# Performance work log

Hardware: AMD Instinct MI355X
Metric: run time of the kernel (lower is better)

The kernel has to match this reference:

```python
import jax, jax.numpy as jnp
import numpy as np
import math

B, H, S, D = 4, 16, 1024, 64
NEG = -1000000000.0

def setup_inputs() -> dict:
    key = jax.random.key(0)
    ks = jax.random.split(key, 6)
    return {
        "query": jax.random.normal(ks[0], (B, H, S, D), dtype=jnp.float32),
        "key": jax.random.normal(ks[1], (B, H, S, D), dtype=jnp.float32),
        "value": jax.random.normal(ks[2], (B, H, S, D), dtype=jnp.float32),
        "head_nums": H,
        "mask": jax.random.randint(ks[3], (B, S), 0, 2, dtype=jnp.int32),
        "topic_query": jax.random.normal(ks[4], (B, S, D), dtype=jnp.float32),
        "topic_key": jax.random.normal(ks[5], (B, S, D), dtype=jnp.float32),
    }

def reference(query, key, value, head_nums, mask, topic_query, topic_key):
    d = query.shape[-1]
    # scores: [B,H,S,S]
    scores = jnp.einsum("bhqd,bhkd->bhqk", query, key) / math.sqrt(d)
    # pairwise mask: [B,S,S] (mask_i * mask_j)
    pair_mask = (mask[:, :, None] * mask[:, None, :]) != 0
    scores = jnp.where(pair_mask[:, None, :, :], scores, NEG)
    # topic modulation: per-token (no head dim), broadcast over heads
    dt = topic_query.shape[-1]
    topic_scores = jnp.einsum("bqd,bkd->bqk", topic_query, topic_key) / math.sqrt(dt)
    topic_scores = jnp.where(pair_mask, topic_scores, 1.0)[:, None, :, :]  # [B,1,S,S]
    topic_probs = jax.nn.softmax(topic_scores, axis=-1)
    scores = scores * topic_probs
    p_attn = jax.nn.softmax(scores, axis=-1)
    out = jnp.einsum("bhqk,bhkd->bhqd", p_attn, value)
    return (out, p_attn)
```

## Files before the change

### kernel.cpp

```cpp
#include <hip/hip_runtime.h>

#define B_ 4
#define H_ 16
#define S_ 1024
#define D_ 64
#define NEGV -1000000000.0f

typedef __bf16 bf16x8 __attribute__((ext_vector_type(8)));
typedef __bf16 bf16x4 __attribute__((ext_vector_type(4)));
typedef float f32x4 __attribute__((ext_vector_type(4)));

__device__ __forceinline__ bf16x8 cvt8(const float* p) {
  float4 x = *(const float4*)p;
  float4 y = *(const float4*)(p + 4);
  bf16x8 f;
  f[0]=(__bf16)x.x; f[1]=(__bf16)x.y; f[2]=(__bf16)x.z; f[3]=(__bf16)x.w;
  f[4]=(__bf16)y.x; f[5]=(__bf16)y.y; f[6]=(__bf16)y.z; f[7]=(__bf16)y.w;
  return f;
}

__global__ __launch_bounds__(256) void prep_kernel(
    const float* __restrict__ K, const float* __restrict__ V,
    __bf16* __restrict__ Kb, __bf16* __restrict__ Vt)
{
  int bid = blockIdx.x;
  int sc = bid & 15;
  int bh = bid >> 4;
  int tid = threadIdx.x;
  __shared__ float s_v[64][65];

  const float* Kc = K + ((size_t)bh*S_ + sc*64)*D_;
  const float* Vc = V + ((size_t)bh*S_ + sc*64)*D_;
  __bf16* Kbc = Kb + ((size_t)bh*S_ + sc*64)*D_;

  {
    const float4* src = (const float4*)Kc + tid*4;
    float4 a = src[0], b = src[1], c = src[2], d = src[3];
    bf16x8 o0, o1;
    o0[0]=(__bf16)a.x; o0[1]=(__bf16)a.y; o0[2]=(__bf16)a.z; o0[3]=(__bf16)a.w;
    o0[4]=(__bf16)b.x; o0[5]=(__bf16)b.y; o0[6]=(__bf16)b.z; o0[7]=(__bf16)b.w;
    o1[0]=(__bf16)c.x; o1[1]=(__bf16)c.y; o1[2]=(__bf16)c.z; o1[3]=(__bf16)c.w;
    o1[4]=(__bf16)d.x; o1[5]=(__bf16)d.y; o1[6]=(__bf16)d.z; o1[7]=(__bf16)d.w;
    *(bf16x8*)(Kbc + tid*16)     = o0;
    *(bf16x8*)(Kbc + tid*16 + 8) = o1;
  }
  for (int i = tid; i < 64*16; i += 256) {
    int r = i >> 4, c4 = i & 15;
    float4 v = ((const float4*)(Vc + (size_t)r*D_))[c4];
    s_v[r][c4*4+0] = v.x; s_v[r][c4*4+1] = v.y;
    s_v[r][c4*4+2] = v.z; s_v[r][c4*4+3] = v.w;
  }
  __syncthreads();
  {
    int d = tid >> 2, seg = tid & 3;
    bf16x8 o0, o1;
    #pragma unroll
    for (int j = 0; j < 8; ++j) o0[j] = (__bf16)s_v[seg*16 + j][d];
    #pragma unroll
    for (int j = 0; j < 8; ++j) o1[j] = (__bf16)s_v[seg*16 + 8 + j][d];
    __bf16* dst = Vt + ((size_t)bh*D_ + d)*S_ + sc*64 + seg*16;
    *(bf16x8*)dst = o0;
    *(bf16x8*)(dst + 8) = o1;
  }
}

__global__ __launch_bounds__(256) void topic_kernel(
    const float* __restrict__ tq, const float* __restrict__ tk,
    const int* __restrict__ mask, float* __restrict__ tp)
{
  int bid0 = blockIdx.x;
  int bid = (bid0 & 7)*32 + (bid0 >> 3);
  int qt = bid & 63, b = bid >> 6;
  int tid = threadIdx.x, wave = tid >> 6, lane = tid & 63;
  int l15 = lane & 15, lhi = lane >> 4;
  __shared__ float2 s_red[4][16];
  __shared__ __align__(16) char s_mem[4*8704];

  const int* mb = mask + b*S_;
  bf16x8 qf[2];
  #pragma unroll
  for (int dc = 0; dc < 2; ++dc)
    qf[dc] = cvt8(tq + ((size_t)b*S_ + qt*16 + l15)*D_ + dc*32 + lhi*8);
  int mq = mb[qt*16 + l15];

  f32x4 sc[16];
  #pragma unroll
  for (int kt = 0; kt < 16; ++kt) {
    int kb = wave*256 + kt*16;
    const float* kr = tk + ((size_t)b*S_ + kb + l15)*D_ + lhi*8;
    bf16x8 k0 = cvt8(kr);
    bf16x8 k1 = cvt8(kr + 32);
    f32x4 acc = {0.f,0.f,0.f,0.f};
    acc = __builtin_amdgcn_mfma_f32_16x16x32_bf16(k0, qf[0], acc, 0, 0, 0);
    acc = __builtin_amdgcn_mfma_f32_16x16x32_bf16(k1, qf[1], acc, 0, 0, 0);
    int4 mk = *(const int4*)(mb + kb + lhi*4);
    sc[kt][0] = (mq && mk.x) ? acc[0]*0.125f : 1.0f;
    sc[kt][1] = (mq && mk.y) ? acc[1]*0.125f : 1.0f;
    sc[kt][2] = (mq && mk.z) ? acc[2]*0.125f : 1.0f;
    sc[kt][3] = (mq && mk.w) ? acc[3]*0.125f : 1.0f;
  }
  float m = -3.4e38f;
  #pragma unroll
  for (int kt = 0; kt < 16; ++kt) {
    #pragma unroll
    for (int i = 0; i < 4; ++i) m = fmaxf(m, sc[kt][i]);
  }
  m = fmaxf(m, __shfl_xor(m, 16));
  m = fmaxf(m, __shfl_xor(m, 32));
  float sum = 0.f;
  #pragma unroll
  for (int kt = 0; kt < 16; ++kt) {
    #pragma unroll
    for (int i = 0; i < 4; ++i) { sc[kt][i] = __expf(sc[kt][i] - m); sum += sc[kt][i]; }
  }
  sum += __shfl_xor(sum, 16);
  sum += __shfl_xor(sum, 32);
  if (lane < 16) s_red[wave][l15] = make_float2(m, sum);
  __syncthreads();
  float M = -3.4e38f;
  #pragma unroll
  for (int w = 0; w < 4; ++w) M = fmaxf(M, s_red[w][l15].x);
  float Z = 0.f;
  #pragma unroll
  for (int w = 0; w < 4; ++w) Z += s_red[w][l15].y * __expf(s_red[w][l15].x - M);
  float scale = __expf(m - M) / Z;

  int mkv[16];
  #pragma unroll
  for (int kt = 0; kt < 16; ++kt) {
    int kb = wave*256 + kt*16;
    int4 mk = *(const int4*)(mb + kb + lhi*4);
    sc[kt][0] *= scale; if (!(mq && mk.x)) sc[kt][0] = -sc[kt][0];
    sc[kt][1] *= scale; if (!(mq && mk.y)) sc[kt][1] = -sc[kt][1];
    sc[kt][2] *= scale; if (!(mq && mk.z)) sc[kt][2] = -sc[kt][2];
    sc[kt][3] *= scale; if (!(mq && mk.w)) sc[kt][3] = -sc[kt][3];
    (void)mkv;
  }

  float* xw = (float*)s_mem + wave*2176;
  float* tpw = tp + ((size_t)b*S_ + qt*16)*S_ + wave*256;
  #pragma unroll
  for (int h = 0; h < 2; ++h) {
    #pragma unroll
    for (int j = 0; j < 8; ++j)
      *(f32x4*)(xw + l15*136 + j*16 + lhi*4) = sc[h*8 + j];
    __syncthreads();
    #pragma unroll
    for (int rr = 0; rr < 8; ++rr) {
      int r = rr*2 + (lane >> 5);
      f32x4 a = *(f32x4*)(xw + r*136 + (lane & 31)*4);
      *(f32x4*)(tpw + (size_t)r*S_ + h*128 + (lane & 31)*4) = a;
    }
    __syncthreads();
  }
}

__global__ __launch_bounds__(256) void attn_kernel(
    const float* __restrict__ Q, const __bf16* __restrict__ Kb,
    const __bf16* __restrict__ Vt, const float* __restrict__ tp,
    float* __restrict__ out, float* __restrict__ pa)
{
  int bid0 = blockIdx.x;
  int bid = (bid0 & 7)*512 + (bid0 >> 3);
  int qt = bid & 63;
  int h  = (bid >> 6) & 15;
  int b  = bid >> 10;
  int tid = threadIdx.x, wave = tid >> 6, lane = tid & 63;
  int l15 = lane & 15, lhi = lane >> 4;

  __shared__ __align__(16) char s_mem[4*8704];
  __shared__ float2 s_red[4][16];

  size_t bh = (size_t)b*H_ + h;
  const __bf16* Kbh = Kb + bh*S_*D_;
  const float* tpb = tp + ((size_t)b*S_ + qt*16 + l15)*S_;

  bf16x8 qf[2];
  #pragma unroll
  for (int dc = 0; dc < 2; ++dc)
    qf[dc] = cvt8(Q + (bh*S_ + qt*16 + l15)*D_ + dc*32 + lhi*8);

  f32x4 sc[16];
  #pragma unroll
  for (int kt = 0; kt < 16; ++kt) {
    int kb = wave*256 + kt*16;
    const __bf16* kr = Kbh + (size_t)(kb + l15)*D_ + lhi*8;
    bf16x8 k0 = *(const bf16x8*)kr;
    bf16x8 k1 = *(const bf16x8*)(kr + 32);
    f32x4 acc = {0.f,0.f,0.f,0.f};
    acc = __builtin_amdgcn_mfma_f32_16x16x32_bf16(k0, qf[0], acc, 0, 0, 0);
    acc = __builtin_amdgcn_mfma_f32_16x16x32_bf16(k1, qf[1], acc, 0, 0, 0);
    float4 t = *(const float4*)(tpb + kb + lhi*4);
    sc[kt][0] = (t.x > 0.f) ? acc[0]*0.125f*t.x : NEGV*(-t.x);
    sc[kt][1] = (t.y > 0.f) ? acc[1]*0.125f*t.y : NEGV*(-t.y);
    sc[kt][2] = (t.z > 0.f) ? acc[2]*0.125f*t.z : NEGV*(-t.z);
    sc[kt][3] = (t.w > 0.f) ? acc[3]*0.125f*t.w : NEGV*(-t.w);
  }

  float m = -3.4e38f;
  #pragma unroll
  for (int kt = 0; kt < 16; ++kt) {
    #pragma unroll
    for (int i = 0; i < 4; ++i) m = fmaxf(m, sc[kt][i]);
  }
  m = fmaxf(m, __shfl_xor(m, 16));
  m = fmaxf(m, __shfl_xor(m, 32));
  float sum = 0.f;
  #pragma unroll
  for (int kt = 0; kt < 16; ++kt) {
    #pragma unroll
    for (int i = 0; i < 4; ++i) { sc[kt][i] = __expf(sc[kt][i] - m); sum += sc[kt][i]; }
  }
  sum += __shfl_xor(sum, 16);
  sum += __shfl_xor(sum, 32);
  if (lane < 16) s_red[wave][l15] = make_float2(m, sum);
  __syncthreads();
  float M = -3.4e38f;
  #pragma unroll
  for (int w = 0; w < 4; ++w) M = fmaxf(M, s_red[w][l15].x);
  float Z = 0.f;
  #pragma unroll
  for (int w = 0; w < 4; ++w) Z += s_red[w][l15].y * __expf(s_red[w][l15].x - M);
  float scale = __expf(m - M) / Z;

  #pragma unroll
  for (int kt = 0; kt < 16; ++kt) {
    #pragma unroll
    for (int i = 0; i < 4; ++i) sc[kt][i] *= scale;
  }

  float* xw = (float*)s_mem + wave*2176;
  float* paw = pa + (bh*S_ + qt*16)*S_ + wave*256;
  #pragma unroll
  for (int hh = 0; hh < 2; ++hh) {
    #pragma unroll
    for (int j = 0; j < 8; ++j)
      *(f32x4*)(xw + l15*136 + j*16 + lhi*4) = sc[hh*8 + j];
    __syncthreads();
    #pragma unroll
    for (int rr = 0; rr < 8; ++rr) {
      int r = rr*2 + (lane >> 5);
      f32x4 a = *(f32x4*)(xw + r*136 + (lane & 31)*4);
      __builtin_nontemporal_store(a, (f32x4*)(paw + (size_t)r*S_ + hh*128 + (lane & 31)*4));
    }
    __syncthreads();
  }

  #pragma unroll
  for (int kt = 0; kt < 16; ++kt) {
    bf16x4 pb;
    pb[0] = (__bf16)sc[kt][0]; pb[1] = (__bf16)sc[kt][1];
    pb[2] = (__bf16)sc[kt][2]; pb[3] = (__bf16)sc[kt][3];
    *(bf16x4*)(s_mem + l15*2048 + ((wave*512 + kt*32 + lhi*8) ^ ((l15 & 7) << 4))) = pb;
  }
  __syncthreads();

  const __bf16* Vh = Vt + (bh*D_ + wave*16 + l15)*S_ + lhi*8;
  f32x4 oacc = {0.f,0.f,0.f,0.f};
  #pragma unroll
  for (int ks = 0; ks < 32; ++ks) {
    bf16x8 a  = *(const bf16x8*)(s_mem + l15*2048 + ((ks*64 + lhi*16) ^ ((l15 & 7) << 4)));
    bf16x8 bv = *(const bf16x8*)(Vh + ks*32);
    oacc = __builtin_amdgcn_mfma_f32_16x16x32_bf16(a, bv, oacc, 0, 0, 0);
  }
  #pragma unroll
  for (int i = 0; i < 4; ++i)
    __builtin_nontemporal_store(oacc[i], out + (bh*S_ + qt*16 + lhi*4 + i)*D_ + wave*16 + l15);
}

extern "C" void kernel_launch(void* const* d_in, const int* in_sizes, int n_in,
                              void* d_out, int out_size, void* d_ws, size_t ws_size,
                              hipStream_t stream) {
  const float* Q    = (const float*)d_in[0];
  const float* K    = (const float*)d_in[1];
  const float* V    = (const float*)d_in[2];
  const int*   mask = (const int*)d_in[4];
  const float* tq   = (const float*)d_in[5];
  const float* tk   = (const float*)d_in[6];

  float*  tp = (float*)d_ws;
  __bf16* Kb = (__bf16*)((char*)d_ws + (size_t)B_*S_*S_*4);
  __bf16* Vt = Kb + (size_t)B_*H_*S_*D_;

  float* outp = (float*)d_out;
  float* pa   = outp + (size_t)B_*H_*S_*D_;

  prep_kernel <<<B_*H_*16, 256, 0, stream>>>(K, V, Kb, Vt);
  topic_kernel<<<B_*64,    256, 0, stream>>>(tq, tk, mask, tp);
  attn_kernel <<<B_*H_*64, 256, 0, stream>>>(Q, Kb, Vt, tp, outp, pa);
}
```

Baseline: 197.6 us.

## Fuse topic softmax into attention kernel, recomputing per head instead of materializing

Drops the separate topic kernel and its 16 MB fp32 topic-probability buffer. Each attention block now recomputes the topic scores and their softmax from bf16 topic keys (converted in prep) and the mask. This removes one launch and the write and 16x re-read of the topic matrix, at the cost of repeating the topic QK^T and softmax once per head. Barriers are also replaced with an lgkmcnt wait plus s_barrier wrapper.

Result: slower. 291.9 us (+47.7%).

```diff
diff --git a/kernel.cpp b/kernel.cpp
--- a/kernel.cpp
+++ b/kernel.cpp
@@ -9,6 +9,15 @@
 typedef __bf16 bf16x8 __attribute__((ext_vector_type(8)));
 typedef __bf16 bf16x4 __attribute__((ext_vector_type(4)));
 typedef float f32x4 __attribute__((ext_vector_type(4)));
+
+#define MFMA16(A, B, C) __builtin_amdgcn_mfma_f32_16x16x32_bf16(A, B, C, 0, 0, 0)
+
+__device__ __forceinline__ void bar_lds() {
+  asm volatile("s_waitcnt lgkmcnt(0)" ::: "memory");
+  __builtin_amdgcn_sched_barrier(0);
+  __builtin_amdgcn_s_barrier();
+  __builtin_amdgcn_sched_barrier(0);
+}
 
 __device__ __forceinline__ bf16x8 cvt8(const float* p) {
   float4 x = *(const float4*)p;
@@ -21,7 +30,8 @@
 
 __global__ __launch_bounds__(256) void prep_kernel(
     const float* __restrict__ K, const float* __restrict__ V,
-    __bf16* __restrict__ Kb, __bf16* __restrict__ Vt)
+    const float* __restrict__ Tk,
+    __bf16* __restrict__ Kb, __bf16* __restrict__ Vt, __bf16* __restrict__ Tkb)
 {
   int bid = blockIdx.x;
   int sc = bid & 15;
@@ -44,6 +54,19 @@
     *(bf16x8*)(Kbc + tid*16)     = o0;
     *(bf16x8*)(Kbc + tid*16 + 8) = o1;
   }
+  if ((bh & 15) == 0) {
+    int b = bh >> 4;
+    const float4* src = (const float4*)(Tk + ((size_t)b*S_ + sc*64)*D_) + tid*4;
+    __bf16* dst = Tkb + ((size_t)b*S_ + sc*64)*D_ + tid*16;
+    float4 a = src[0], bb = src[1], c = src[2], d = src[3];
+    bf16x8 o0, o1;
+    o0[0]=(__bf16)a.x;  o0[1]=(__bf16)a.y;  o0[2]=(__bf16)a.z;  o0[3]=(__bf16)a.w;
+    o0[4]=(__bf16)bb.x; o0[5]=(__bf16)bb.y; o0[6]=(__bf16)bb.z; o0[7]=(__bf16)bb.w;
+    o1[0]=(__bf16)c.x;  o1[1]=(__bf16)c.y;  o1[2]=(__bf16)c.z;  o1[3]=(__bf16)c.w;
+    o1[4]=(__bf16)d.x;  o1[5]=(__bf16)d.y;  o1[6]=(__bf16)d.z;  o1[7]=(__bf16)d.w;
+    *(bf16x8*)dst       = o0;
+    *(bf16x8*)(dst + 8) = o1;
+  }
   for (int i = tid; i < 64*16; i += 256) {
     int r = i >> 4, c4 = i & 15;
     float4 v = ((const float4*)(Vc + (size_t)r*D_))[c4];
@@ -64,100 +87,10 @@
   }
 }
 
-__global__ __launch_bounds__(256) void topic_kernel(
-    const float* __restrict__ tq, const float* __restrict__ tk,
-    const int* __restrict__ mask, float* __restrict__ tp)
-{
-  int bid0 = blockIdx.x;
-  int bid = (bid0 & 7)*32 + (bid0 >> 3);
-  int qt = bid & 63, b = bid >> 6;
-  int tid = threadIdx.x, wave = tid >> 6, lane = tid & 63;
-  int l15 = lane & 15, lhi = lane >> 4;
-  __shared__ float2 s_red[4][16];
-  __shared__ __align__(16) char s_mem[4*8704];
-
-  const int* mb = mask + b*S_;
-  bf16x8 qf[2];
-  #pragma unroll
-  for (int dc = 0; dc < 2; ++dc)
-    qf[dc] = cvt8(tq + ((size_t)b*S_ + qt*16 + l15)*D_ + dc*32 + lhi*8);
-  int mq = mb[qt*16 + l15];
-
-  f32x4 sc[16];
-  #pragma unroll
-  for (int kt = 0; kt < 16; ++kt) {
-    int kb = wave*256 + kt*16;
-    const float* kr = tk + ((size_t)b*S_ + kb + l15)*D_ + lhi*8;
-    bf16x8 k0 = cvt8(kr);
-    bf16x8 k1 = cvt8(kr + 32);
-    f32x4 acc = {0.f,0.f,0.f,0.f};
-    acc = __builtin_amdgcn_mfma_f32_16x16x32_bf16(k0, qf[0], acc, 0, 0, 0);
-    acc = __builtin_amdgcn_mfma_f32_16x16x32_bf16(k1, qf[1], acc, 0, 0, 0);
-    int4 mk = *(const int4*)(mb + kb + lhi*4);
-    sc[kt][0] = (mq && mk.x) ? acc[0]*0.125f : 1.0f;
-    sc[kt][1] = (mq && mk.y) ? acc[1]*0.125f : 1.0f;
-    sc[kt][2] = (mq && mk.z) ? acc[2]*0.125f : 1.0f;
-    sc[kt][3] = (mq && mk.w) ? acc[3]*0.125f : 1.0f;
-  }
-  float m = -3.4e38f;
-  #pragma unroll
-  for (int kt = 0; kt < 16; ++kt) {
-    #pragma unroll
-    for (int i = 0; i < 4; ++i) m = fmaxf(m, sc[kt][i]);
-  }
-  m = fmaxf(m, __shfl_xor(m, 16));
-  m = fmaxf(m, __shfl_xor(m, 32));
-  float sum = 0.f;
-  #pragma unroll
-  for (int kt = 0; kt < 16; ++kt) {
-    #pragma unroll
-    for (int i = 0; i < 4; ++i) { sc[kt][i] = __expf(sc[kt][i] - m); sum += sc[kt][i]; }
-  }
-  sum += __shfl_xor(sum, 16);
-  sum += __shfl_xor(sum, 32);
-  if (lane < 16) s_red[wave][l15] = make_float2(m, sum);
-  __syncthreads();
-  float M = -3.4e38f;
-  #pragma unroll
-  for (int w = 0; w < 4; ++w) M = fmaxf(M, s_red[w][l15].x);
-  float Z = 0.f;
-  #pragma unroll
-  for (int w = 0; w < 4; ++w) Z += s_red[w][l15].y * __expf(s_red[w][l15].x - M);
-  float scale = __expf(m - M) / Z;
-
-  int mkv[16];
-  #pragma unroll
-  for (int kt = 0; kt < 16; ++kt) {
-    int kb = wave*256 + kt*16;
-    int4 mk = *(const int4*)(mb + kb + lhi*4);
-    sc[kt][0] *= scale; if (!(mq && mk.x)) sc[kt][0] = -sc[kt][0];
-    sc[kt][1] *= scale; if (!(mq && mk.y)) sc[kt][1] = -sc[kt][1];
-    sc[kt][2] *= scale; if (!(mq && mk.z)) sc[kt][2] = -sc[kt][2];
-    sc[kt][3] *= scale; if (!(mq && mk.w)) sc[kt][3] = -sc[kt][3];
-    (void)mkv;
-  }
-
-  float* xw = (float*)s_mem + wave*2176;
-  float* tpw = tp + ((size_t)b*S_ + qt*16)*S_ + wave*256;
-  #pragma unroll
-  for (int h = 0; h < 2; ++h) {
-    #pragma unroll
-    for (int j = 0; j < 8; ++j)
-      *(f32x4*)(xw + l15*136 + j*16 + lhi*4) = sc[h*8 + j];
-    __syncthreads();
-    #pragma unroll
-    for (int rr = 0; rr < 8; ++rr) {
-      int r = rr*2 + (lane >> 5);
-      f32x4 a = *(f32x4*)(xw + r*136 + (lane & 31)*4);
-      *(f32x4*)(tpw + (size_t)r*S_ + h*128 + (lane & 31)*4) = a;
-    }
-    __syncthreads();
-  }
-}
-
 __global__ __launch_bounds__(256) void attn_kernel(
     const float* __restrict__ Q, const __bf16* __restrict__ Kb,
-    const __bf16* __restrict__ Vt, const float* __restrict__ tp,
+    const __bf16* __restrict__ Vt, const __bf16* __restrict__ Tkb,
+    const float* __restrict__ tq, const int* __restrict__ mask,
     float* __restrict__ out, float* __restrict__ pa)
 {
   int bid0 = blockIdx.x;
@@ -169,65 +102,117 @@
   int l15 = lane & 15, lhi = lane >> 4;
 
   __shared__ __align__(16) char s_mem[4*8704];
-  __shared__ float2 s_red[4][16];
+  __shared__ float2 s_redA[4][16];
+  __shared__ float2 s_redB[4][16];
 
   size_t bh = (size_t)b*H_ + h;
   const __bf16* Kbh = Kb + bh*S_*D_;
-  const float* tpb = tp + ((size_t)b*S_ + qt*16 + l15)*S_;
-
-  bf16x8 qf[2];
-  #pragma unroll
-  for (int dc = 0; dc < 2; ++dc)
-    qf[dc] = cvt8(Q + (bh*S_ + qt*16 + l15)*D_ + dc*32 + lhi*8);
-
-  f32x4 sc[16];
-  #pragma unroll
-  for (int kt = 0; kt < 16; ++kt) {
-    int kb = wave*256 + kt*16;
-    const __bf16* kr = Kbh + (size_t)(kb + l15)*D_ + lhi*8;
-    bf16x8 k0 = *(const bf16x8*)kr;
-    bf16x8 k1 = *(const bf16x8*)(kr + 32);
-    f32x4 acc = {0.f,0.f,0.f,0.f};
-    acc = __builtin_amdgcn_mfma_f32_16x16x32_bf16(k0, qf[0], acc, 0, 0, 0);
-    acc = __builtin_amdgcn_mfma_f32_16x16x32_bf16(k1, qf[1], acc, 0, 0, 0);
-    float4 t = *(const float4*)(tpb + kb + lhi*4);
-    sc[kt][0] = (t.x > 0.f) ? acc[0]*0.125f*t.x : NEGV*(-t.x);
-    sc[kt][1] = (t.y > 0.f) ? acc[1]*0.125f*t.y : NEGV*(-t.y);
-    sc[kt][2] = (t.z > 0.f) ? acc[2]*0.125f*t.z : NEGV*(-t.z);
-    sc[kt][3] = (t.w > 0.f) ? acc[3]*0.125f*t.w : NEGV*(-t.w);
-  }
-
+  const __bf16* Tkh = Tkb + (size_t)b*S_*D_;
+  const int* mb = mask + b*S_;
+  int mq = mb[qt*16 + l15];
+
+  f32x4 ts[16];
+  {
+    bf16x8 tqf[2];
+    #pragma unroll
+    for (int dc = 0; dc < 2; ++dc)
+      tqf[dc] = cvt8(tq + ((size_t)b*S_ + qt*16 + l15)*D_ + dc*32 + lhi*8);
+    #pragma unroll
+    for (int kt = 0; kt < 16; ++kt) {
+      int kb = wave*256 + kt*16;
+      const __bf16* tkr = Tkh + (size_t)(kb + l15)*D_ + lhi*8;
+      bf16x8 t0 = *(const bf16x8*)tkr;
+      bf16x8 t1 = *(const bf16x8*)(tkr + 32);
+      f32x4 acc = {0.f,0.f,0.f,0.f};
+      acc = MFMA16(t0, tqf[0], acc);
+      acc = MFMA16(t1, tqf[1], acc);
+      int4 mk = *(const int4*)(mb + kb + lhi*4);
+      ts[kt][0] = (mq && mk.x) ? acc[0]*0.125f : 1.0f;
+      ts[kt][1] = (mq && mk.y) ? acc[1]*0.125f : 1.0f;
+      ts[kt][2] = (mq && mk.z) ? acc[2]*0.125f : 1.0f;
+      ts[kt][3] = (mq && mk.w) ? acc[3]*0.125f : 1.0f;
+    }
+  }
+  float scale_t;
+  {
+    float m = -3.4e38f;
+    #pragma unroll
+    for (int kt = 0; kt < 16; ++kt)
+      #pragma unroll
+      for (int i = 0; i < 4; ++i) m = fmaxf(m, ts[kt][i]);
+    m = fmaxf(m, __shfl_xor(m, 16));
+    m = fmaxf(m, __shfl_xor(m, 32));
+    float sum = 0.f;
+    #pragma unroll
+    for (int kt = 0; kt < 16; ++kt)
+      #pragma unroll
+      for (int i = 0; i < 4; ++i) { ts[kt][i] = __expf(ts[kt][i] - m); sum += ts[kt][i]; }
+    sum += __shfl_xor(sum, 16);
+    sum += __shfl_xor(sum, 32);
+    if (lane < 16) s_redA[wave][l15] = make_float2(m, sum);
+    bar_lds();
+    float M = -3.4e38f;
+    #pragma unroll
+    for (int w = 0; w < 4; ++w) M = fmaxf(M, s_redA[w][l15].x);
+    float Z = 0.f;
+    #pragma unroll
+    for (int w = 0; w < 4; ++w) Z += s_redA[w][l15].y * __expf(s_redA[w][l15].x - M);
+    scale_t = __expf(m - M) / Z;
+  }
+
+  {
+    bf16x8 qf[2];
+    #pragma unroll
+    for (int dc = 0; dc < 2; ++dc)
+      qf[dc] = cvt8(Q + (bh*S_ + qt*16 + l15)*D_ + dc*32 + lhi*8);
+    #pragma unroll
+    for (int kt = 0; kt < 16; ++kt) {
+      int kb = wave*256 + kt*16;
+      const __bf16* kr = Kbh + (size_t)(kb + l15)*D_ + lhi*8;
+      bf16x8 k0 = *(const bf16x8*)kr;
+      bf16x8 k1 = *(const bf16x8*)(kr + 32);
+      f32x4 acc = {0.f,0.f,0.f,0.f};
+      acc = MFMA16(k0, qf[0], acc);
+      acc = MFMA16(k1, qf[1], acc);
+      int4 mk = *(const int4*)(mb + kb + lhi*4);
+      float t0 = ts[kt][0]*scale_t, t1 = ts[kt][1]*scale_t;
+      float t2 = ts[kt][2]*scale_t, t3 = ts[kt][3]*scale_t;
+      ts[kt][0] = (mq && mk.x) ? acc[0]*0.125f*t0 : NEGV*t0;
+      ts[kt][1] = (mq && mk.y) ? acc[1]*0.125f*t1 : NEGV*t1;
+      ts[kt][2] = (mq && mk.z) ? acc[2]*0.125f*t2 : NEGV*t2;
+      ts[kt][3] = (mq && mk.w) ? acc[3]*0.125f*t3 : NEGV*t3;
+    }
+  }
+
+  float scale;
   float m = -3.4e38f;
   #pragma unroll
-  for (int kt = 0; kt < 16; ++kt) {
-    #pragma unroll
-    for (int i = 0; i < 4; ++i) m = fmaxf(m, sc[kt][i]);
-  }
+  for (int kt = 0; kt < 16; ++kt)
+    #pragma unroll
+    for (int i = 0; i < 4; ++i) m = fmaxf(m, ts[kt][i]);
   m = fmaxf(m, __shfl_xor(m, 16));
   m = fmaxf(m, __shfl_xor(m, 32));
   float sum = 0.f;
   #pragma unroll
-  for (int kt = 0; kt < 16; ++kt) {
-    #pragma unroll
-    for (int i = 0; i < 4; ++i) { sc[kt][i] = __expf(sc[kt][i] - m); sum += sc[kt][i]; }
-  }
+  for (int kt = 0; kt < 16; ++kt)
+    #pragma unroll
+    for (int i = 0; i < 4; ++i) { ts[kt][i] = __expf(ts[kt][i] - m); sum += ts[kt][i]; }
   sum += __shfl_xor(sum, 16);
   sum += __shfl_xor(sum, 32);
-  if (lane < 16) s_red[wave][l15] = make_float2(m, sum);
-  __syncthreads();
+  if (lane < 16) s_redB[wave][l15] = make_float2(m, sum);
+  bar_lds();
   float M = -3.4e38f;
   #pragma unroll
-  for (int w = 0; w < 4; ++w) M = fmaxf(M, s_red[w][l15].x);
+  for (int w = 0; w < 4; ++w) M = fmaxf(M, s_redB[w][l15].x);
   float Z = 0.f;
   #pragma unroll
-  for (int w = 0; w < 4; ++w) Z += s_red[w][l15].y * __expf(s_red[w][l15].x - M);
-  float scale = __expf(m - M) / Z;
-
-  #pragma unroll
-  for (int kt = 0; kt < 16; ++kt) {
-    #pragma unroll
-    for (int i = 0; i < 4; ++i) sc[kt][i] *= scale;
-  }
+  for (int w = 0; w < 4; ++w) Z += s_redB[w][l15].y * __expf(s_redB[w][l15].x - M);
+  scale = __expf(m - M) / Z;
+
+  #pragma unroll
+  for (int kt = 0; kt < 16; ++kt)
+    #pragma unroll
+    for (int i = 0; i < 4; ++i) ts[kt][i] *= scale;
 
   float* xw = (float*)s_mem + wave*2176;
   float* paw = pa + (bh*S_ + qt*16)*S_ + wave*256;
@@ -235,25 +220,25 @@
   for (int hh = 0; hh < 2; ++hh) {
     #pragma unroll
     for (int j = 0; j < 8; ++j)
-      *(f32x4*)(xw + l15*136 + j*16 + lhi*4) = sc[hh*8 + j];
-    __syncthreads();
+      *(f32x4*)(xw + l15*136 + j*16 + lhi*4) = ts[hh*8 + j];
+    bar_lds();
     #pragma unroll
     for (int rr = 0; rr < 8; ++rr) {
       int r = rr*2 + (lane >> 5);
       f32x4 a = *(f32x4*)(xw + r*136 + (lane & 31)*4);
       __builtin_nontemporal_store(a, (f32x4*)(paw + (size_t)r*S_ + hh*128 + (lane & 31)*4));
     }
-    __syncthreads();
+    bar_lds();
   }
 
   #pragma unroll
   for (int kt = 0; kt < 16; ++kt) {
     bf16x4 pb;
-    pb[0] = (__bf16)sc[kt][0]; pb[1] = (__bf16)sc[kt][1];
-    pb[2] = (__bf16)sc[kt][2]; pb[3] = (__bf16)sc[kt][3];
+    pb[0] = (__bf16)ts[kt][0]; pb[1] = (__bf16)ts[kt][1];
+    pb[2] = (__bf16)ts[kt][2]; pb[3] = (__bf16)ts[kt][3];
     *(bf16x4*)(s_mem + l15*2048 + ((wave*512 + kt*32 + lhi*8) ^ ((l15 & 7) << 4))) = pb;
   }
-  __syncthreads();
+  bar_lds();
 
   const __bf16* Vh = Vt + (bh*D_ + wave*16 + l15)*S_ + lhi*8;
   f32x4 oacc = {0.f,0.f,0.f,0.f};
@@ -261,7 +246,7 @@
   for (int ks = 0; ks < 32; ++ks) {
     bf16x8 a  = *(const bf16x8*)(s_mem + l15*2048 + ((ks*64 + lhi*16) ^ ((l15 & 7) << 4)));
     bf16x8 bv = *(const bf16x8*)(Vh + ks*32);
-    oacc = __builtin_amdgcn_mfma_f32_16x16x32_bf16(a, bv, oacc, 0, 0, 0);
+    oacc = MFMA16(a, bv, oacc);
   }
   #pragma unroll
   for (int i = 0; i < 4; ++i)
@@ -278,14 +263,13 @@
   const float* tq   = (const float*)d_in[5];
   const float* tk   = (const float*)d_in[6];
 
-  float*  tp = (float*)d_ws;
-  __bf16* Kb = (__bf16*)((char*)d_ws + (size_t)B_*S_*S_*4);
-  __bf16* Vt = Kb + (size_t)B_*H_*S_*D_;
+  __bf16* Kb  = (__bf16*)d_ws;
+  __bf16* Vt  = Kb + (size_t)B_*H_*S_*D_;
+  __bf16* Tkb = Vt + (size_t)B_*H_*S_*D_;
 
   float* outp = (float*)d_out;
   float* pa   = outp + (size_t)B_*H_*S_*D_;
 
-  prep_kernel <<<B_*H_*16, 256, 0, stream>>>(K, V, Kb, Vt);
-  topic_kernel<<<B_*64,    256, 0, stream>>>(tq, tk, mask, tp);
-  attn_kernel <<<B_*H_*64, 256, 0, stream>>>(Q, Kb, Vt, tp, outp, pa);
-}
+  prep_kernel <<<B_*H_*16, 256, 0, stream>>>(K, V, tk, Kb, Vt, Tkb);
+  attn_kernel <<<B_*H_*64, 256, 0, stream>>>(Q, Kb, Vt, Tkb, tq, mask, outp, pa);
+}
```
